# Optimization experiments

Measured on AMD Instinct MI355X. Metric: run time of the kernel, lower is better.

Reference implementation:

```python
import jax, jax.numpy as jnp
import numpy as np

B, T, D, H = 256, 2048, 64, 64

def setup_inputs() -> dict:
    key = jax.random.key(0)
    ks = jax.random.split(key, 9)
    s_in = 1.0 / np.sqrt(D)
    s_rec = 1.0 / np.sqrt(H)
    return {
        "lstm_input": jax.random.normal(ks[0], (B, T, D), dtype=jnp.float32),
        "inputs_state": jax.random.normal(ks[1], (B, H), dtype=jnp.float32),
        # LSTM kernel/recurrent_kernel/bias, Keras gate order [i, f, c, o]
        "W": jax.random.normal(ks[2], (D, 4 * H), dtype=jnp.float32) * s_in,
        "U": jax.random.normal(ks[3], (H, 4 * H), dtype=jnp.float32) * s_rec,
        "b": jax.random.normal(ks[4], (4 * H,), dtype=jnp.float32) * 0.05,
        # Dense(1) heads
        "w_gamma": jax.random.normal(ks[5], (H, 1), dtype=jnp.float32) * s_rec,
        "b_gamma": jax.random.normal(ks[6], (1,), dtype=jnp.float32) * 0.05,
        "w_beta": jax.random.normal(ks[7], (H, 1), dtype=jnp.float32) * s_rec,
        "b_beta": jax.random.normal(ks[8], (1,), dtype=jnp.float32) * 0.05,
    }

def reference(lstm_input, inputs_state, W, U, b, w_gamma, b_gamma, w_beta, b_beta):
    # Keras LSTM(64, activation='sigmoid'): recurrent_activation=sigmoid (gates),
    # activation=sigmoid (candidate + cell output, replacing the usual tanh).
    # get_initial_state(inputs_state) -> zero h0/c0 (only batch size is used).
    sig = jax.nn.sigmoid
    # Precompute input projections for all timesteps: [B,T,4H]
    xz = jnp.einsum('btd,dg->btg', lstm_input, W) + b

    def step(carry, z_t):
        h, c = carry
        z = z_t + h @ U  # [B,4H]
        i, f, g, o = jnp.split(z, 4, axis=-1)
        c = sig(f) * c + sig(i) * sig(g)
        h = sig(o) * sig(c)
        return (h, c), None

    h0 = jnp.zeros((lstm_input.shape[0], H), dtype=lstm_input.dtype)
    c0 = jnp.zeros_like(h0)
    (h, _), _ = jax.lax.scan(step, (h0, c0), jnp.swapaxes(xz, 0, 1))

    gamma = h @ w_gamma + b_gamma  # [B,1]
    beta = h @ w_beta + b_beta     # [B,1]
    return (gamma, beta)
```

## Files before the change

### kernel.cpp

```cpp
#include <hip/hip_runtime.h>


typedef _Float16 f16;
typedef f16  half8 __attribute__((ext_vector_type(8)));
typedef __fp16 fp16x2 __attribute__((ext_vector_type(2)));
typedef float f32x4 __attribute__((ext_vector_type(4)));

constexpr int Bsz = 256;
constexpr int Tn  = 2048;
constexpr int Dn  = 64;
constexpr int G4  = 256;

__global__ __launch_bounds__(256, 1) void lstm_film_mfma(
    const float* __restrict__ x,
    const float* __restrict__ W,
    const float* __restrict__ U,
    const float* __restrict__ bias,
    const float* __restrict__ wg, const float* __restrict__ bgam,
    const float* __restrict__ wb, const float* __restrict__ bbet,
    float* __restrict__ out)
{
    __shared__ __align__(16) char hbuf[2][128];
    __shared__ __align__(16) float c_lds[64];

    const int tid  = threadIdx.x;
    const int w    = tid >> 6;
    const int l    = tid & 63;
    const int lrow = l & 15;
    const int kgrp = l >> 4;

    const float NK = -1.44269504f;

    half8 Bf[4][4];
#pragma unroll
    for (int kf = 0; kf < 4; ++kf) {
        const float* M = (kf < 2) ? U : W;
        const int krow0 = (kf & 1) * 32 + kgrp * 8;
#pragma unroll
        for (int q = 0; q < 4; ++q) {
            const int col = q * 64 + w * 16 + lrow;
#pragma unroll
            for (int j = 0; j < 8; ++j)
                Bf[kf][q][j] = (f16)(M[(krow0 + j) * G4 + col] * NK);
        }
    }
    f32x4 bqv[4];
#pragma unroll
    for (int q = 0; q < 4; ++q) {
        const float b = bias[q * 64 + w * 16 + lrow] * NK;
        bqv[q] = f32x4{b, b, b, b};
    }
    const f32x4 ZV = {0.f, 0.f, 0.f, 0.f};

    if (tid < 16) ((uint4*)hbuf)[tid] = uint4{0, 0, 0, 0};
    if (tid < 64) c_lds[tid] = 0.0f;
    float c = 0.0f;

    const float* xlane = x + ((size_t)blockIdx.x * Tn + lrow) * Dn + kgrp * 8;
    const int rdH0 = kgrp * 16;
    const int rdH1 = kgrp * 16 + 64;
    const int wrH  = (w * 16 + lrow) * 2;
    const int cidx = w * 16 + lrow;

    const float wgj = wg[l], wbj = wb[l];
    const float bg0 = bgam[0], bb0 = bbet[0];

    __syncthreads();

    union U16 { fp16x2 p[4]; half8 h8; };
    U16 u0, u1;
    float4 R[4];
    f32x4 qA0, qA1, qA2, qA3, qB0, qB1, qB2, qB3;

#define XL(T0) do { const float* p_ = xlane + (size_t)(T0) * Dn;             \
        R[0] = *(const float4*)(p_);      R[1] = *(const float4*)(p_ + 4);   \
        R[2] = *(const float4*)(p_ + 32); R[3] = *(const float4*)(p_ + 36);  \
    } while (0)

#define CVT0 do {                                                            \
        u0.p[0] = __builtin_amdgcn_cvt_pkrtz(R[0].x, R[0].y);                \
        u0.p[1] = __builtin_amdgcn_cvt_pkrtz(R[0].z, R[0].w);                \
        u0.p[2] = __builtin_amdgcn_cvt_pkrtz(R[1].x, R[1].y);                \
        u0.p[3] = __builtin_amdgcn_cvt_pkrtz(R[1].z, R[1].w); } while (0)
#define CVT1 do {                                                            \
        u1.p[0] = __builtin_amdgcn_cvt_pkrtz(R[2].x, R[2].y);                \
        u1.p[1] = __builtin_amdgcn_cvt_pkrtz(R[2].z, R[2].w);                \
        u1.p[2] = __builtin_amdgcn_cvt_pkrtz(R[3].x, R[3].y);                \
        u1.p[3] = __builtin_amdgcn_cvt_pkrtz(R[3].z, R[3].w); } while (0)

#define MFM __builtin_amdgcn_mfma_f32_16x16x32_f16

#define HSTEP(S, Q, ...) do {                                                \
        asm volatile("s_waitcnt lgkmcnt(0)" ::: "memory");                   \
        __builtin_amdgcn_s_barrier();                                        \
        asm volatile("" ::: "memory");                                       \
        const char* hb_ = hbuf[(S) & 1];                                     \
        half8 ah0 = *(const half8*)(hb_ + rdH0);                             \
        half8 ah1 = *(const half8*)(hb_ + rdH1);                             \
        if (((S) & 3) == 0) c = c_lds[cidx];                                 \
        f32x4 a0 = MFM(ah0, Bf[0][0], bqv[0], 0, 0, 0);                      \
        f32x4 a1 = MFM(ah0, Bf[0][1], bqv[1], 0, 0, 0);                      \
        f32x4 a2 = MFM(ah0, Bf[0][2], bqv[2], 0, 0, 0);                      \
        f32x4 a3 = MFM(ah0, Bf[0][3], bqv[3], 0, 0, 0);                      \
        a0 = MFM(ah1, Bf[1][0], a0, 0, 0, 0);                                \
        a1 = MFM(ah1, Bf[1][1], a1, 0, 0, 0);                                \
        a2 = MFM(ah1, Bf[1][2], a2, 0, 0, 0);                                \
        a3 = MFM(ah1, Bf[1][3], a3, 0, 0, 0);                                \
        __VA_ARGS__                                                          \
        const float zi = Q##0[(S) & 3] + a0[(S) & 3];                        \
        const float zf = Q##1[(S) & 3] + a1[(S) & 3];                        \
        const float zg = Q##2[(S) & 3] + a2[(S) & 3];                        \
        const float zo = Q##3[(S) & 3] + a3[(S) & 3];                        \
        const float ei = __builtin_amdgcn_exp2f(zi);                         \
        const float ef = __builtin_amdgcn_exp2f(zf);                         \
        const float eg = __builtin_amdgcn_exp2f(zg);                         \
        const float eo = __builtin_amdgcn_exp2f(zo);                         \
        const float sf  = __builtin_amdgcn_rcpf(1.0f + ef);                  \
        const float sig = __builtin_amdgcn_rcpf((1.0f + ei) * (1.0f + eg));  \
        c = fmaf(sf, c, sig);                                                \
        const float ec = __builtin_amdgcn_exp2f(c * NK);                     \
        const float hh = __builtin_amdgcn_rcpf((1.0f + eo) * (1.0f + ec));   \
        if (kgrp == ((S) >> 2)) {                                            \
            *(f16*)(hbuf[((S) & 1) ^ 1] + wrH) = (f16)hh;                    \
            if (((S) & 3) == 3) c_lds[cidx] = c;                             \
        }                                                                    \
    } while (0)

#define BLOCK16(QC, QN, TNX)                                                 \
        HSTEP(0, QC);  HSTEP(1, QC);  HSTEP(2, QC);  HSTEP(3, QC);           \
        HSTEP(4, QC);  HSTEP(5, QC);  HSTEP(6, QC);  HSTEP(7, QC);           \
        HSTEP(8, QC,  CVT0; QN##0 = MFM(u0.h8, Bf[2][0], ZV, 0, 0, 0); );    \
        HSTEP(9, QC,        QN##1 = MFM(u0.h8, Bf[2][1], ZV, 0, 0, 0); );    \
        HSTEP(10, QC,       QN##2 = MFM(u0.h8, Bf[2][2], ZV, 0, 0, 0); );    \
        HSTEP(11, QC,       QN##3 = MFM(u0.h8, Bf[2][3], ZV, 0, 0, 0); );    \
        HSTEP(12, QC, CVT1; QN##0 = MFM(u1.h8, Bf[3][0], QN##0, 0, 0, 0); ); \
        HSTEP(13, QC,       QN##1 = MFM(u1.h8, Bf[3][1], QN##1, 0, 0, 0);    \
                            XL(TNX); );                                      \
        HSTEP(14, QC,       QN##2 = MFM(u1.h8, Bf[3][2], QN##2, 0, 0, 0); ); \
        HSTEP(15, QC,       QN##3 = MFM(u1.h8, Bf[3][3], QN##3, 0, 0, 0); );

    XL(0);
    CVT0; CVT1;
    qA0 = MFM(u0.h8, Bf[2][0], ZV, 0, 0, 0);
    qA1 = MFM(u0.h8, Bf[2][1], ZV, 0, 0, 0);
    qA2 = MFM(u0.h8, Bf[2][2], ZV, 0, 0, 0);
    qA3 = MFM(u0.h8, Bf[2][3], ZV, 0, 0, 0);
    qA0 = MFM(u1.h8, Bf[3][0], qA0, 0, 0, 0);
    qA1 = MFM(u1.h8, Bf[3][1], qA1, 0, 0, 0);
    qA2 = MFM(u1.h8, Bf[3][2], qA2, 0, 0, 0);
    qA3 = MFM(u1.h8, Bf[3][3], qA3, 0, 0, 0);
    XL(16);

    for (int tb = 0; tb < Tn / 16; tb += 2) {
        int t2 = (tb + 2) * 16; if (t2 > Tn - 16) t2 = Tn - 16;
        int t3 = (tb + 3) * 16; if (t3 > Tn - 16) t3 = Tn - 16;
        BLOCK16(qA, qB, t2)
        BLOCK16(qB, qA, t3)
    }
#undef BLOCK16
#undef HSTEP
#undef MFM
#undef CVT0
#undef CVT1
#undef XL

    __syncthreads();

    if (w == 0) {
        const float hv = (float)*(const f16*)(hbuf[0] + l * 2);
        float vg = hv * wgj, vb = hv * wbj;
#pragma unroll
        for (int off = 32; off > 0; off >>= 1) {
            vg += __shfl_xor(vg, off, 64);
            vb += __shfl_xor(vb, off, 64);
        }
        if (l == 0) {
            out[blockIdx.x]       = vg + bg0;
            out[Bsz + blockIdx.x] = vb + bb0;
        }
    }
}

extern "C" void kernel_launch(void* const* d_in, const int* in_sizes, int n_in,
                              void* d_out, int out_size, void* d_ws, size_t ws_size,
                              hipStream_t stream) {
    const float* x    = (const float*)d_in[0];
    const float* W    = (const float*)d_in[2];
    const float* U    = (const float*)d_in[3];
    const float* bias = (const float*)d_in[4];
    const float* wg   = (const float*)d_in[5];
    const float* bgam = (const float*)d_in[6];
    const float* wb   = (const float*)d_in[7];
    const float* bbet = (const float*)d_in[8];
    float* out = (float*)d_out;

    lstm_film_mfma<<<Bsz, 256, 0, stream>>>(x, W, U, bias,
                                            wg, bgam, wb, bbet, out);
}
```

Baseline: 456.0 us.

## Pack two independent batch rows per 512-thread block

Each block now runs two batch rows with eight waves, four per row, and each row group keeps its own h and c buffers in LDS. The grid is halved to 128 blocks. The intent is to interleave two independent recurrence chains on one CU so their latencies overlap. The cost is that the per-step s_barrier now waits on all eight waves, which couples the two chains, and only half of the 256 CUs are used.

After: 582.2 us. 1.28x slower.

```diff
diff --git a/kernel.cpp b/kernel.cpp
--- a/kernel.cpp
+++ b/kernel.cpp
@@ -11,7 +11,7 @@
 constexpr int Dn  = 64;
 constexpr int G4  = 256;
 
-__global__ __launch_bounds__(256, 1) void lstm_film_mfma(
+__global__ __launch_bounds__(512, 1) void lstm_film_mfma(
     const float* __restrict__ x,
     const float* __restrict__ W,
     const float* __restrict__ U,
@@ -20,11 +20,13 @@
     const float* __restrict__ wb, const float* __restrict__ bbet,
     float* __restrict__ out)
 {
-    __shared__ __align__(16) char hbuf[2][128];
-    __shared__ __align__(16) float c_lds[64];
+    __shared__ __align__(16) char hbuf[2][2][128];
+    __shared__ __align__(16) float c_lds[2][64];
 
     const int tid  = threadIdx.x;
     const int w    = tid >> 6;
+    const int grp  = w >> 2;
+    const int wl   = w & 3;
     const int l    = tid & 63;
     const int lrow = l & 15;
     const int kgrp = l >> 4;
@@ -38,7 +40,7 @@
         const int krow0 = (kf & 1) * 32 + kgrp * 8;
 #pragma unroll
         for (int q = 0; q < 4; ++q) {
-            const int col = q * 64 + w * 16 + lrow;
+            const int col = q * 64 + wl * 16 + lrow;
 #pragma unroll
             for (int j = 0; j < 8; ++j)
                 Bf[kf][q][j] = (f16)(M[(krow0 + j) * G4 + col] * NK);
@@ -47,20 +49,24 @@
     f32x4 bqv[4];
 #pragma unroll
     for (int q = 0; q < 4; ++q) {
-        const float b = bias[q * 64 + w * 16 + lrow] * NK;
+        const float b = bias[q * 64 + wl * 16 + lrow] * NK;
         bqv[q] = f32x4{b, b, b, b};
     }
     const f32x4 ZV = {0.f, 0.f, 0.f, 0.f};
 
-    if (tid < 16) ((uint4*)hbuf)[tid] = uint4{0, 0, 0, 0};
-    if (tid < 64) c_lds[tid] = 0.0f;
+    if (tid < 32) ((uint4*)hbuf)[tid] = uint4{0, 0, 0, 0};
+    if (tid < 128) ((float*)c_lds)[tid] = 0.0f;
     float c = 0.0f;
 
-    const float* xlane = x + ((size_t)blockIdx.x * Tn + lrow) * Dn + kgrp * 8;
+    const int batch = blockIdx.x * 2 + grp;
+    const float* xlane = x + ((size_t)batch * Tn + lrow) * Dn + kgrp * 8;
+    const char* hb0 = hbuf[grp][0];
+    const char* hb1 = hbuf[grp][1];
     const int rdH0 = kgrp * 16;
     const int rdH1 = kgrp * 16 + 64;
-    const int wrH  = (w * 16 + lrow) * 2;
-    const int cidx = w * 16 + lrow;
+    const int wrH  = (wl * 16 + lrow) * 2;
+    float* cg = c_lds[grp];
+    const int cidx = wl * 16 + lrow;
 
     const float wgj = wg[l], wbj = wb[l];
     const float bg0 = bgam[0], bb0 = bbet[0];
@@ -94,10 +100,10 @@
         asm volatile("s_waitcnt lgkmcnt(0)" ::: "memory");                   \
         __builtin_amdgcn_s_barrier();                                        \
         asm volatile("" ::: "memory");                                       \
-        const char* hb_ = hbuf[(S) & 1];                                     \
+        const char* hb_ = ((S) & 1) ? hb1 : hb0;                             \
         half8 ah0 = *(const half8*)(hb_ + rdH0);                             \
         half8 ah1 = *(const half8*)(hb_ + rdH1);                             \
-        if (((S) & 3) == 0) c = c_lds[cidx];                                 \
+        if (((S) & 3) == 0) c = cg[cidx];                                    \
         f32x4 a0 = MFM(ah0, Bf[0][0], bqv[0], 0, 0, 0);                      \
         f32x4 a1 = MFM(ah0, Bf[0][1], bqv[1], 0, 0, 0);                      \
         f32x4 a2 = MFM(ah0, Bf[0][2], bqv[2], 0, 0, 0);                      \
@@ -121,8 +127,9 @@
         const float ec = __builtin_amdgcn_exp2f(c * NK);                     \
         const float hh = __builtin_amdgcn_rcpf((1.0f + eo) * (1.0f + ec));   \
         if (kgrp == ((S) >> 2)) {                                            \
-            *(f16*)(hbuf[((S) & 1) ^ 1] + wrH) = (f16)hh;                    \
-            if (((S) & 3) == 3) c_lds[cidx] = c;                             \
+            char* ho_ = (char*)(((S) & 1) ? hb0 : hb1);                      \
+            *(f16*)(ho_ + wrH) = (f16)hh;                                    \
+            if (((S) & 3) == 3) cg[cidx] = c;                                \
         }                                                                    \
     } while (0)
 
@@ -166,8 +173,8 @@
 
     __syncthreads();
 
-    if (w == 0) {
-        const float hv = (float)*(const f16*)(hbuf[0] + l * 2);
+    if (wl == 0) {
+        const float hv = (float)*(const f16*)(hbuf[grp][0] + l * 2);
         float vg = hv * wgj, vb = hv * wbj;
 #pragma unroll
         for (int off = 32; off > 0; off >>= 1) {
@@ -175,8 +182,8 @@
             vb += __shfl_xor(vb, off, 64);
         }
         if (l == 0) {
-            out[blockIdx.x]       = vg + bg0;
-            out[Bsz + blockIdx.x] = vb + bb0;
+            out[batch]       = vg + bg0;
+            out[Bsz + batch] = vb + bb0;
         }
     }
 }
@@ -194,6 +201,6 @@
     const float* bbet = (const float*)d_in[8];
     float* out = (float*)d_out;
 
-    lstm_film_mfma<<<Bsz, 256, 0, stream>>>(x, W, U, bias,
-                                            wg, bgam, wb, bbet, out);
+    lstm_film_mfma<<<Bsz / 2, 512, 0, stream>>>(x, W, U, bias,
+                                                wg, bgam, wb, bbet, out);
 }
```
